# Kernel optimization log

Measured on AMD Instinct MI355X. Metric: run time of the kernel, lower is better.

## Reference

```python
import jax, jax.numpy as jnp
import numpy as np

B, P, ENC = 128, 196, 2048
D, A, ED, V, L = 512, 512, 512, 10000, 20


def setup_inputs() -> dict:
    key = jax.random.key(0)
    ks = jax.random.split(key, 24)
    s = 0.02
    inp = {
        'encoder_out': jax.random.normal(ks[0], (B, P, ENC), jnp.float32),
        'captions': jax.random.randint(ks[1], (B, L), 0, V),
        'caption_len': jax.random.randint(ks[2], (B,), 2, L + 1).at[0].set(L),
        # embedding (uniform(-0.1, 0.1) per init_weights)
        'emb_w': jax.random.uniform(ks[3], (V, ED), jnp.float32, -0.1, 0.1),
        # LSTMCell: input = ED + ENC, hidden = D, gates order i,f,g,o
        'Wih': jax.random.normal(ks[4], (4 * D, ED + ENC), jnp.float32) * s,
        'Whh': jax.random.normal(ks[5], (4 * D, D), jnp.float32) * s,
        'bih': jax.random.normal(ks[6], (4 * D,), jnp.float32) * s,
        'bhh': jax.random.normal(ks[7], (4 * D,), jnp.float32) * s,
        # init hidden state projections
        'h0_w': jax.random.normal(ks[8], (D, ENC), jnp.float32) * s,
        'h0_b': jnp.zeros((D,), jnp.float32),
        'c0_w': jax.random.normal(ks[9], (D, ENC), jnp.float32) * s,
        'c0_b': jnp.zeros((D,), jnp.float32),
        # gate D -> ENC
        'gate_w': jax.random.normal(ks[10], (ENC, D), jnp.float32) * s,
        'gate_b': jnp.zeros((ENC,), jnp.float32),
        # output projection D -> V (uniform(-0.1,0.1), bias 0 per init_weights)
        'lin_w': jax.random.uniform(ks[11], (V, D), jnp.float32, -0.1, 0.1),
        'lin_b': jnp.zeros((V,), jnp.float32),
        # attention network
        'ea_w': jax.random.normal(ks[12], (A, ENC), jnp.float32) * s,
        'ea_b': jnp.zeros((A,), jnp.float32),
        'da_w': jax.random.normal(ks[13], (A, D), jnp.float32) * s,
        'da_b': jnp.zeros((A,), jnp.float32),
        'fa_w': jax.random.normal(ks[14], (1, A), jnp.float32) * s,
        'fa_b': jnp.zeros((1,), jnp.float32),
    }
    return inp


def reference(encoder_out, captions, caption_len, emb_w, Wih, Whh, bih, bhh,
              h0_w, h0_b, c0_w, c0_b, gate_w, gate_b, lin_w, lin_b,
              ea_w, ea_b, da_w, da_b, fa_w, fa_b):
    # sort by caption length descending (as in torch .sort(descending=True))
    order = jnp.argsort(-caption_len)
    cap_len = caption_len[order]
    enc = encoder_out[order]            # [B, P, ENC]
    caps = captions[order]              # [B, L]
    dec_len = cap_len - 1               # per-example decode lengths

    emb = emb_w[caps]                   # [B, L, ED]
    mean_enc = enc.mean(axis=1)         # [B, ENC]
    h0 = mean_enc @ h0_w.T + h0_b       # [B, D]
    c0 = mean_enc @ c0_w.T + c0_b
    att1 = enc @ ea_w.T + ea_b          # [B, P, A] precomputed encoder attention

    T = caps.shape[1] - 1               # static max decode steps (caption_len[0]=L)

    def step(carry, i):
        h, c = carry
        # Bahdanau attention
        att2 = h @ da_w.T + da_b                                   # [B, A]
        e = (jax.nn.relu(att1 + att2[:, None, :]) @ fa_w.T + fa_b)[..., 0]  # [B, P]
        alpha = jax.nn.softmax(e, axis=1)
        awe = jnp.einsum('bp,bpe->be', alpha, enc)                 # [B, ENC]
        g = jax.nn.sigmoid(h @ gate_w.T + gate_b)
        awe = g * awe
        # LSTMCell
        x = jnp.concatenate([emb[:, i, :], awe], axis=1)           # [B, ED+ENC]
        gates = x @ Wih.T + bih + h @ Whh.T + bhh                  # [B, 4D]
        gi, gf, gg, go = jnp.split(gates, 4, axis=1)
        c_new = jax.nn.sigmoid(gf) * c + jax.nn.sigmoid(gi) * jnp.tanh(gg)
        h_new = jax.nn.sigmoid(go) * jnp.tanh(c_new)
        active = (i < dec_len)[:, None]                            # ragged mask
        # inactive rows keep old state (matches h[:batch_size_i] slicing)
        h2 = jnp.where(active, h_new, h)
        c2 = jnp.where(active, c_new, c)
        # dropout is identity in eval; output projection masked to zeros
        pred = jnp.where(active, h_new @ lin_w.T + lin_b, 0.0)     # [B, V]
        alpha = jnp.where(active, alpha, 0.0)
        return (h2, c2), (pred, alpha)

    (_, _), (preds, alphas) = jax.lax.scan(step, (h0, c0), jnp.arange(T))
    pred = jnp.swapaxes(preds, 0, 1)     # [B, T, V]
    alphas = jnp.swapaxes(alphas, 0, 1)  # [B, T, P]
    return pred, caps, dec_len, alphas, order
```

## Files before the change

kernel.cpp:

```cpp
#include <hip/hip_runtime.h>
#include <hip/hip_bf16.h>
#include <math.h>

#define Bn 128
#define Pn 196
#define ENCn 2048
#define Dn 512
#define An 512
#define EDn 512
#define Vn 10000
#define Ln 20
#define Tn 19

typedef short v8s __attribute__((ext_vector_type(8)));
typedef float v4f __attribute__((ext_vector_type(4)));

__device__ __forceinline__ float sigf(float x){ return 1.f/(1.f+__expf(-x)); }
__device__ __forceinline__ unsigned short f2bf(float f){
  unsigned u = __float_as_uint(f);
  return (unsigned short)((u + 0x7FFFu + ((u>>16)&1u)) >> 16);
}
__device__ __forceinline__ float bf2f(unsigned short h){
  return __uint_as_float(((unsigned)h)<<16);
}


__global__ void k_order(const int* __restrict__ caption_len,
                        const int* __restrict__ captions,
                        int* __restrict__ order_i, int* __restrict__ declen_i,
                        int* __restrict__ caps_s,
                        float* __restrict__ out_caps, float* __restrict__ out_declen,
                        float* __restrict__ out_order)
{
  __shared__ int lens[Bn];
  int b = threadIdx.x;
  lens[b] = caption_len[b];
  __syncthreads();
  int lb = lens[b];
  int r = 0;
  for (int j = 0; j < Bn; ++j) {
    int lj = lens[j];
    r += (int)((lj > lb) || (lj == lb && j < b));
  }
  order_i[r] = b;
  declen_i[r] = lb - 1;
  out_order[r] = (float)b;
  out_declen[r] = (float)(lb - 1);
  for (int t = 0; t < Ln; ++t) {
    int cv = captions[b*Ln + t];
    caps_s[r*Ln + t] = cv;
    out_caps[r*Ln + t] = (float)cv;
  }
}

__global__ void k_setup_bias(const float* __restrict__ bih, const float* __restrict__ bhh,
                             const float* __restrict__ da_b, const float* __restrict__ gate_b,
                             const float* __restrict__ h0_b, const float* __restrict__ c0_b,
                             float* __restrict__ bsum_r, float* __restrict__ dg_b,
                             float* __restrict__ hc_b)
{
  int i = blockIdx.x*256 + threadIdx.x;
  if (i < 2048) {
    int d = i >> 2, g = i & 3;
    bsum_r[i] = bih[g*512+d] + bhh[g*512+d];
  }
  if (i < 2560) dg_b[i] = (i < 512) ? da_b[i] : gate_b[i-512];
  if (i < 1024) hc_b[i] = (i < 512) ? h0_b[i] : c0_b[i-512];
}

__global__ void k_cvt(const float* __restrict__ src, unsigned short* __restrict__ dst, int n)
{
  int i = (blockIdx.x*256 + threadIdx.x)*4;
  if (i < n) {
    float4 v = *(const float4*)(src + i);
    dst[i+0]=f2bf(v.x); dst[i+1]=f2bf(v.y); dst[i+2]=f2bf(v.z); dst[i+3]=f2bf(v.w);
  }
}

__global__ void k_wcat(const float* __restrict__ Wih, const float* __restrict__ Whh,
                       unsigned short* __restrict__ dst)
{
  int i = (blockIdx.x*256 + threadIdx.x)*4;
  if (i >= 2048*3072) return;
  int rp = i/3072, j = i - rp*3072;
  int d = rp >> 2, g = rp & 3;
  int r = g*512 + d;
  const float* s = (j < 2560) ? (Wih + (size_t)r*2560 + j) : (Whh + (size_t)r*512 + (j-2560));
  float4 v = *(const float4*)s;
  dst[i+0]=f2bf(v.x); dst[i+1]=f2bf(v.y); dst[i+2]=f2bf(v.z); dst[i+3]=f2bf(v.w);
}

__global__ void k_cvt_enc(const float* __restrict__ enc, const int* __restrict__ order_i,
                          unsigned short* __restrict__ dst)
{
  int id = blockIdx.x;
  int b = id / Pn, p = id - b*Pn;
  const float* src = enc + ((size_t)order_i[b]*Pn + p)*ENCn;
  unsigned short* d = dst + (size_t)id*ENCn;
  int i = threadIdx.x*8;
  float4 v0 = *(const float4*)(src+i), v1 = *(const float4*)(src+i+4);
  d[i+0]=f2bf(v0.x); d[i+1]=f2bf(v0.y); d[i+2]=f2bf(v0.z); d[i+3]=f2bf(v0.w);
  d[i+4]=f2bf(v1.x); d[i+5]=f2bf(v1.y); d[i+6]=f2bf(v1.z); d[i+7]=f2bf(v1.w);
}

__global__ void k_mean(const unsigned short* __restrict__ enc_bf,
                       unsigned short* __restrict__ mean_bf)
{
  int b = blockIdx.x;
  const unsigned short* eb = enc_bf + (size_t)b*Pn*ENCn;
  for (int e = threadIdx.x; e < ENCn; e += 256) {
    float s = 0.f;
    for (int p = 0; p < Pn; ++p) s += bf2f(eb[(size_t)p*ENCn + e]);
    mean_bf[b*ENCn + e] = f2bf(s * (1.f/196.f));
  }
}

__global__ void k_zero(uint4* __restrict__ p, int n)
{
  int i = blockIdx.x*256 + threadIdx.x;
  if (i < n) p[i] = uint4{0,0,0,0};
}

__global__ void k_emb_all(const int* __restrict__ caps_s, const float* __restrict__ emb_w,
                          unsigned short* __restrict__ xh_all)
{
  int id = blockIdx.x; int t = id >> 7, b = id & 127;
  int tok = caps_s[b*Ln + t];
  const float* src = emb_w + (size_t)tok*EDn;
  unsigned short* d = xh_all + ((size_t)t*Bn + b)*3072;
  int i = threadIdx.x*2;
  float2 v = *(const float2*)(src+i);
  d[i] = f2bf(v.x); d[i+1] = f2bf(v.y);
}

__global__ void k_h2bf(const float* __restrict__ hc, float* __restrict__ c,
                       unsigned short* __restrict__ h_bf, unsigned short* __restrict__ xh_all)
{
  int b = blockIdx.x, d = threadIdx.x;
  float hv = hc[b*1024 + d];
  float cv = hc[b*1024 + 512 + d];
  c[b*Dn + d] = cv;
  unsigned short hb = f2bf(hv);
  h_bf[b*Dn + d] = hb;
  xh_all[(size_t)b*3072 + 2560 + d] = hb;
}

template<int MODE, bool OUT_BF16>
__global__ __launch_bounds__(256) void k_mfma_gemm(
    const unsigned short* __restrict__ Aw, const unsigned short* __restrict__ Bw,
    const float* __restrict__ bias, void* __restrict__ Cp,
    int M, int N, int K, size_t ldc,
    const int* __restrict__ actlen, int t)
{
  __shared__ unsigned short smA[2][4096];
  __shared__ unsigned short smB[2][4096];
  const int tid = threadIdx.x;
  int bm0, bn0;
  if constexpr (MODE == 1) {
    int id = blockIdx.x;
    int xcd = id & 7, j = id >> 3;
    int g = j >> 6, rem = j & 63;
    int panel, col;
    if (g < 6) { panel = xcd*49 + g*8 + (rem & 7); col = rem >> 3; }
    else       { panel = xcd*49 + 48;              col = rem; }
    bm0 = panel*64; bn0 = col*64;
  } else {
    bm0 = blockIdx.y*64; bn0 = blockIdx.x*64;
  }

  if (MODE == 0 && actlen && actlen[bm0] <= t) return;

  const int lane = tid & 63, w = tid >> 6;
  const int wr = w >> 1, wc = w & 1;
  const int lrow = lane & 15, kq = lane >> 4;

  v4f acc[2][2];
  #pragma unroll
  for (int i=0;i<2;++i)
    #pragma unroll
    for (int j=0;j<2;++j) acc[i][j] = (v4f)0.f;

  const int nt = K >> 6;

  auto stage = [&](int buf, int k0) {
    #pragma unroll
    for (int it = 0; it < 2; ++it) {
      int s = it*256 + tid;
      int row = s >> 3;
      int kb  = (s & 7) ^ (row & 7);
      {
        const v8s v = *(const v8s*)(Aw + (size_t)(bm0+row)*K + k0 + kb*8);
        *(v8s*)&smA[buf][s*8] = v;
      }
      {
        int gn = bn0 + row; if (gn >= N) gn = N-1;
        const v8s v = *(const v8s*)(Bw + (size_t)gn*K + k0 + kb*8);
        *(v8s*)&smB[buf][s*8] = v;
      }
    }
  };

  auto compute = [&](int buf) {
    #pragma unroll
    for (int kc = 0; kc < 2; ++kc) {
      v8s aF[2], bF[2];
      #pragma unroll
      for (int mi = 0; mi < 2; ++mi) {
        int row = wr*32 + mi*16 + lrow;
        int kb = kc*4 + kq;
        aF[mi] = *(const v8s*)&smA[buf][row*64 + ((kb ^ (row&7))<<3)];
      }
      #pragma unroll
      for (int ni = 0; ni < 2; ++ni) {
        int row = wc*32 + ni*16 + lrow;
        int kb = kc*4 + kq;
        bF[ni] = *(const v8s*)&smB[buf][row*64 + ((kb ^ (row&7))<<3)];
      }
      #pragma unroll
      for (int mi = 0; mi < 2; ++mi)
        #pragma unroll
        for (int ni = 0; ni < 2; ++ni)
          acc[mi][ni] = __builtin_amdgcn_mfma_f32_16x16x32_bf16(aF[mi], bF[ni], acc[mi][ni], 0, 0, 0);
    }
  };

  stage(0, 0);
  __syncthreads();
  for (int tk = 0; tk < nt; ++tk) {
    if (tk + 1 < nt) stage((tk+1)&1, (tk+1)<<6);
    compute(tk&1);
    __syncthreads();
  }

  #pragma unroll
  for (int mi=0; mi<2; ++mi)
    #pragma unroll
    for (int ni=0; ni<2; ++ni) {
      #pragma unroll
      for (int r=0; r<4; ++r) {
        int m = bm0 + wr*32 + mi*16 + kq*4 + r;
        int n = bn0 + wc*32 + ni*16 + lrow;
        if (m < M && n < N) {
          float v = acc[mi][ni][r] + (bias ? bias[n] : 0.f);
          if constexpr (OUT_BF16) ((unsigned short*)Cp)[(size_t)m*ldc + n] = f2bf(v);
          else ((float*)Cp)[(size_t)m*ldc + n] = v;
        }
      }
    }
}

__global__ __launch_bounds__(256) void k_gates_lstm(
    const unsigned short* __restrict__ Aw, const unsigned short* __restrict__ Bw,
    const float* __restrict__ bias,
    float* __restrict__ c, unsigned short* __restrict__ h_bf,
    unsigned short* __restrict__ h_all, unsigned short* __restrict__ xh_all,
    const int* __restrict__ declen_i, int t)
{
  __shared__ unsigned short smA[2][4096];
  __shared__ unsigned short smB[2][4096];
  __shared__ float smC[64][65];
  const int tid = threadIdx.x;
  const int bm0 = blockIdx.y*64, bn0 = blockIdx.x*64;
  if (declen_i[bm0] <= t) return;

  const int lane = tid & 63, w = tid >> 6;
  const int wr = w >> 1, wc = w & 1;
  const int lrow = lane & 15, kq = lane >> 4;
  const int K = 3072;

  v4f acc[2][2];
  #pragma unroll
  for (int i=0;i<2;++i)
    #pragma unroll
    for (int j=0;j<2;++j) acc[i][j] = (v4f)0.f;

  auto stage = [&](int buf, int k0) {
    #pragma unroll
    for (int it = 0; it < 2; ++it) {
      int s = it*256 + tid;
      int row = s >> 3;
      int kb  = (s & 7) ^ (row & 7);
      *(v8s*)&smA[buf][s*8] = *(const v8s*)(Aw + (size_t)(bm0+row)*K + k0 + kb*8);
      *(v8s*)&smB[buf][s*8] = *(const v8s*)(Bw + (size_t)(bn0+row)*K + k0 + kb*8);
    }
  };
  auto compute = [&](int buf) {
    #pragma unroll
    for (int kc = 0; kc < 2; ++kc) {
      v8s aF[2], bF[2];
      #pragma unroll
      for (int mi = 0; mi < 2; ++mi) {
        int row = wr*32 + mi*16 + lrow;
        int kb = kc*4 + kq;
        aF[mi] = *(const v8s*)&smA[buf][row*64 + ((kb ^ (row&7))<<3)];
      }
      #pragma unroll
      for (int ni = 0; ni < 2; ++ni) {
        int row = wc*32 + ni*16 + lrow;
        int kb = kc*4 + kq;
        bF[ni] = *(const v8s*)&smB[buf][row*64 + ((kb ^ (row&7))<<3)];
      }
      #pragma unroll
      for (int mi = 0; mi < 2; ++mi)
        #pragma unroll
        for (int ni = 0; ni < 2; ++ni)
          acc[mi][ni] = __builtin_amdgcn_mfma_f32_16x16x32_bf16(aF[mi], bF[ni], acc[mi][ni], 0, 0, 0);
    }
  };

  stage(0, 0);
  __syncthreads();
  const int nt = K >> 6;
  for (int tk = 0; tk < nt; ++tk) {
    if (tk + 1 < nt) stage((tk+1)&1, (tk+1)<<6);
    compute(tk&1);
    __syncthreads();
  }

  #pragma unroll
  for (int mi=0; mi<2; ++mi)
    #pragma unroll
    for (int ni=0; ni<2; ++ni)
      #pragma unroll
      for (int r=0; r<4; ++r) {
        int ml = wr*32 + mi*16 + kq*4 + r;
        int nl = wc*32 + ni*16 + lrow;
        smC[ml][nl] = acc[mi][ni][r] + bias[bn0 + nl];
      }
  __syncthreads();

  for (int idx = tid; idx < 1024; idx += 256) {
    int ml = idx >> 4, dl = idx & 15;
    int b = bm0 + ml;
    if (t < declen_i[b]) {
      int dg = (bn0 >> 2) + dl;
      float gi = smC[ml][dl*4+0];
      float gf = smC[ml][dl*4+1];
      float gg = smC[ml][dl*4+2];
      float go = smC[ml][dl*4+3];
      float cv = c[b*Dn + dg];
      float cn = sigf(gf)*cv + sigf(gi)*tanhf(gg);
      float hn = sigf(go)*tanhf(cn);
      c[b*Dn + dg] = cn;
      unsigned short hb = f2bf(hn);
      h_bf[b*Dn + dg] = hb;
      h_all[((size_t)t*Bn + b)*Dn + dg] = hb;
      if (t + 1 < Tn)
        xh_all[((size_t)(t+1)*Bn + b)*3072 + 2560 + dg] = hb;
    }
  }
}

__global__ __launch_bounds__(256) void k_pred(
    const unsigned short* __restrict__ Aw, const unsigned short* __restrict__ Bw,
    const float* __restrict__ bias, float* __restrict__ out_pred,
    const int* __restrict__ declen_i)
{
  __shared__ unsigned short smA[2][4096];
  __shared__ unsigned short smB[2][4096];
  const int tid = threadIdx.x;
  const int bm0 = blockIdx.y*64, bn0 = blockIdx.x*64;
  const int t0 = bm0 >> 7, b0 = bm0 & 127;

  if (declen_i[b0] <= t0) {
    for (int i = tid; i < 4096; i += 256) {
      int ml = i >> 6, nl = i & 63;
      int n = bn0 + nl;
      if (n < Vn) {
        int m = bm0 + ml;
        out_pred[((size_t)(m & 127)*Tn + (m >> 7))*Vn + n] = 0.f;
      }
    }
    return;
  }

  const int lane = tid & 63, w = tid >> 6;
  const int wr = w >> 1, wc = w & 1;
  const int lrow = lane & 15, kq = lane >> 4;
  const int K = 512;

  v4f acc[2][2];
  #pragma unroll
  for (int i=0;i<2;++i)
    #pragma unroll
    for (int j=0;j<2;++j) acc[i][j] = (v4f)0.f;

  auto stage = [&](int buf, int k0) {
    #pragma unroll
    for (int it = 0; it < 2; ++it) {
      int s = it*256 + tid;
      int row = s >> 3;
      int kb  = (s & 7) ^ (row & 7);
      *(v8s*)&smA[buf][s*8] = *(const v8s*)(Aw + (size_t)(bm0+row)*K + k0 + kb*8);
      {
        int gn = bn0 + row; if (gn >= Vn) gn = Vn-1;
        *(v8s*)&smB[buf][s*8] = *(const v8s*)(Bw + (size_t)gn*K + k0 + kb*8);
      }
    }
  };
  auto compute = [&](int buf) {
    #pragma unroll
    for (int kc = 0; kc < 2; ++kc) {
      v8s aF[2], bF[2];
      #pragma unroll
      for (int mi = 0; mi < 2; ++mi) {
        int row = wr*32 + mi*16 + lrow;
        int kb = kc*4 + kq;
        aF[mi] = *(const v8s*)&smA[buf][row*64 + ((kb ^ (row&7))<<3)];
      }
      #pragma unroll
      for (int ni = 0; ni < 2; ++ni) {
        int row = wc*32 + ni*16 + lrow;
        int kb = kc*4 + kq;
        bF[ni] = *(const v8s*)&smB[buf][row*64 + ((kb ^ (row&7))<<3)];
      }
      #pragma unroll
      for (int mi = 0; mi < 2; ++mi)
        #pragma unroll
        for (int ni = 0; ni < 2; ++ni)
          acc[mi][ni] = __builtin_amdgcn_mfma_f32_16x16x32_bf16(aF[mi], bF[ni], acc[mi][ni], 0, 0, 0);
    }
  };

  stage(0, 0);
  __syncthreads();
  const int nt = K >> 6;
  for (int tk = 0; tk < nt; ++tk) {
    if (tk + 1 < nt) stage((tk+1)&1, (tk+1)<<6);
    compute(tk&1);
    __syncthreads();
  }

  #pragma unroll
  for (int mi=0; mi<2; ++mi)
    #pragma unroll
    for (int ni=0; ni<2; ++ni)
      #pragma unroll
      for (int r=0; r<4; ++r) {
        int m = bm0 + wr*32 + mi*16 + kq*4 + r;
        int n = bn0 + wc*32 + ni*16 + lrow;
        if (n < Vn) {
          int b = m & 127, tt = m >> 7;
          float v = (tt < declen_i[b]) ? (acc[mi][ni][r] + bias[n]) : 0.f;
          out_pred[((size_t)b*Tn + tt)*Vn + n] = v;
        }
      }
}

__global__ __launch_bounds__(256) void k_esm(
    const unsigned short* __restrict__ att1, const float* __restrict__ att2g,
    const float* __restrict__ fa_w, const float* __restrict__ fa_b,
    float* __restrict__ alpha, float* __restrict__ out_alph,
    const int* __restrict__ declen_i, int t)
{
  int b = blockIdx.x;
  int tid = threadIdx.x;
  if (t >= declen_i[b]) {
    if (tid < Pn)
      out_alph[(size_t)b*Tn*Pn + (size_t)t*Pn + tid] = 0.f;
    return;
  }
  __shared__ float a2s[An];
  __shared__ float fws[An];
  __shared__ float es[Pn];
  __shared__ float wred[4];
  __shared__ float wsum[4];
  for (int i = tid; i < An; i += 256) { a2s[i] = att2g[(size_t)b*2560 + i]; fws[i] = fa_w[i]; }
  __syncthreads();
  int lane = tid & 63, w = tid >> 6;
  if (tid < Pn) {
    const unsigned short* row = att1 + ((size_t)b*Pn + tid)*An;
    float s = 0.f;
    #pragma unroll 4
    for (int kb = 0; kb < 64; ++kb) {
      const v8s vv = *(const v8s*)(row + kb*8);
      #pragma unroll
      for (int j = 0; j < 8; ++j) {
        int a = kb*8 + j;
        float v = bf2f((unsigned short)vv[j]) + a2s[a];
        s += fmaxf(v, 0.f) * fws[a];
      }
    }
    es[tid] = s + fa_b[0];
  }
  __syncthreads();
  float m = -1e30f;
  for (int p = tid; p < Pn; p += 256) m = fmaxf(m, es[p]);
  for (int off = 32; off; off >>= 1) m = fmaxf(m, __shfl_down(m, off));
  if (lane == 0) wred[w] = m;
  __syncthreads();
  m = fmaxf(fmaxf(wred[0], wred[1]), fmaxf(wred[2], wred[3]));
  float s = 0.f;
  for (int p = tid; p < Pn; p += 256) { float ev = __expf(es[p] - m); es[p] = ev; s += ev; }
  for (int off = 32; off; off >>= 1) s += __shfl_down(s, off);
  if (lane == 0) wsum[w] = s;
  __syncthreads();
  s = wsum[0] + wsum[1] + wsum[2] + wsum[3];
  float inv = 1.f / s;
  for (int p = tid; p < Pn; p += 256) {
    float al = es[p] * inv;
    alpha[b*Pn + p] = al;
    out_alph[(size_t)b*Tn*Pn + (size_t)t*Pn + p] = al;
  }
}

__global__ __launch_bounds__(256) void k_awe_gate(
    const unsigned short* __restrict__ enc_bf,
    const float* __restrict__ alpha, const float* __restrict__ att2g,
    unsigned short* __restrict__ xh_t, const int* __restrict__ declen_i, int t)
{
  int b = blockIdx.y;
  if (t >= declen_i[b]) return;
  __shared__ float als[Pn];
  __shared__ float red[8][256];
  int tid = threadIdx.x;
  if (tid < Pn) als[tid] = alpha[b*Pn + tid];
  __syncthreads();
  int e0 = blockIdx.x*256;
  int ec = tid & 31, ps = tid >> 5;
  const unsigned short* eb = enc_bf + (size_t)b*Pn*ENCn + e0 + ec*8;
  float s[8] = {};
  for (int p = ps; p < Pn; p += 8) {
    v8s v = *(const v8s*)(eb + (size_t)p*ENCn);
    float a = als[p];
    #pragma unroll
    for (int j = 0; j < 8; ++j) s[j] += a * bf2f((unsigned short)v[j]);
  }
  #pragma unroll
  for (int j = 0; j < 8; ++j) red[ps][ec*8+j] = s[j];
  __syncthreads();
  {
    int e = tid;
    float tsum = 0.f;
    #pragma unroll
    for (int k = 0; k < 8; ++k) tsum += red[k][e];
    int eg = e0 + e;
    float g = sigf(att2g[(size_t)b*2560 + 512 + eg]);
    xh_t[(size_t)b*3072 + 512 + eg] = f2bf(g*tsum);
  }
}


extern "C" void kernel_launch(void* const* d_in, const int* in_sizes, int n_in,
                              void* d_out, int out_size, void* d_ws, size_t ws_size,
                              hipStream_t stream)
{
  const float* enc     = (const float*)d_in[0];
  const int*   captions= (const int*)d_in[1];
  const int*   cap_len = (const int*)d_in[2];
  const float* emb_w   = (const float*)d_in[3];
  const float* Wih     = (const float*)d_in[4];
  const float* Whh     = (const float*)d_in[5];
  const float* bih     = (const float*)d_in[6];
  const float* bhh     = (const float*)d_in[7];
  const float* h0_w    = (const float*)d_in[8];
  const float* h0_b    = (const float*)d_in[9];
  const float* c0_w    = (const float*)d_in[10];
  const float* c0_b    = (const float*)d_in[11];
  const float* gate_w  = (const float*)d_in[12];
  const float* gate_b  = (const float*)d_in[13];
  const float* lin_w   = (const float*)d_in[14];
  const float* lin_b   = (const float*)d_in[15];
  const float* ea_w    = (const float*)d_in[16];
  const float* ea_b    = (const float*)d_in[17];
  const float* da_w    = (const float*)d_in[18];
  const float* da_b    = (const float*)d_in[19];
  const float* fa_w    = (const float*)d_in[20];
  const float* fa_b    = (const float*)d_in[21];

  float* out = (float*)d_out;
  float* out_pred   = out;
  float* out_caps   = out + (size_t)Bn*Tn*Vn;
  float* out_declen = out_caps + Bn*Ln;
  float* out_alph   = out_declen + Bn;
  float* out_order  = out_alph + (size_t)Bn*Tn*Pn;

  char* wp = (char*)d_ws;
  auto alloc = [&](size_t bytes)->void* {
    void* p = (void*)wp; wp += (bytes + 255) & ~(size_t)255; return p;
  };
  int*   order_i  = (int*)alloc(Bn*4);
  int*   declen_i = (int*)alloc(Bn*4);
  int*   caps_s   = (int*)alloc(Bn*Ln*4);
  unsigned short* enc_bf  = (unsigned short*)alloc((size_t)Bn*Pn*ENCn*2);
  unsigned short* mean_bf = (unsigned short*)alloc((size_t)Bn*ENCn*2);
  float* hc       = (float*)alloc((size_t)Bn*1024*4);
  float* c        = (float*)alloc((size_t)Bn*Dn*4);
  unsigned short* h_bf   = (unsigned short*)alloc((size_t)Bn*Dn*2);
  unsigned short* h_all  = (unsigned short*)alloc((size_t)Tn*Bn*Dn*2);
  unsigned short* xh_all = (unsigned short*)alloc((size_t)Tn*Bn*3072*2);
  unsigned short* att1   = (unsigned short*)alloc((size_t)Bn*Pn*An*2);
  float* att2g    = (float*)alloc((size_t)Bn*2560*4);
  float* alpha    = (float*)alloc((size_t)Bn*Pn*4);
  unsigned short* ea_bf   = (unsigned short*)alloc((size_t)An*ENCn*2);
  unsigned short* lin_bf  = (unsigned short*)alloc((size_t)Vn*Dn*2);
  unsigned short* h0c0_bf = (unsigned short*)alloc((size_t)1024*ENCn*2);
  unsigned short* dg_bf   = (unsigned short*)alloc((size_t)2560*Dn*2);
  unsigned short* wcat_bf = (unsigned short*)alloc((size_t)2048*3072*2);
  float* bsum = (float*)alloc(2048*4);
  float* dg_b = (float*)alloc(2560*4);
  float* hc_b = (float*)alloc(1024*4);

  k_order<<<1,128,0,stream>>>(cap_len, captions, order_i, declen_i, caps_s,
                              out_caps, out_declen, out_order);
  k_setup_bias<<<10,256,0,stream>>>(bih, bhh, da_b, gate_b, h0_b, c0_b, bsum, dg_b, hc_b);
  k_cvt<<<(An*ENCn/4+255)/256,256,0,stream>>>(ea_w, ea_bf, An*ENCn);
  k_cvt<<<(Vn*Dn/4+255)/256,256,0,stream>>>(lin_w, lin_bf, Vn*Dn);
  k_cvt<<<(Dn*ENCn/4+255)/256,256,0,stream>>>(h0_w, h0c0_bf, Dn*ENCn);
  k_cvt<<<(Dn*ENCn/4+255)/256,256,0,stream>>>(c0_w, h0c0_bf + (size_t)512*ENCn, Dn*ENCn);
  k_cvt<<<(An*Dn/4+255)/256,256,0,stream>>>(da_w, dg_bf, An*Dn);
  k_cvt<<<(ENCn*Dn/4+255)/256,256,0,stream>>>(gate_w, dg_bf + (size_t)512*Dn, ENCn*Dn);
  k_wcat<<<(2048*3072/4+255)/256,256,0,stream>>>(Wih, Whh, wcat_bf);
  k_cvt_enc<<<Bn*Pn,256,0,stream>>>(enc, order_i, enc_bf);
  k_mean<<<Bn,256,0,stream>>>(enc_bf, mean_bf);
  k_zero<<<((int)((size_t)Tn*Bn*3072*2/16)+255)/256,256,0,stream>>>(
      (uint4*)xh_all, (int)((size_t)Tn*Bn*3072*2/16));
  k_emb_all<<<Tn*Bn,256,0,stream>>>(caps_s, emb_w, xh_all);

  k_mfma_gemm<0,false><<<dim3(16,2),256,0,stream>>>(
      mean_bf, h0c0_bf, hc_b, hc, Bn, 1024, ENCn, 1024, nullptr, 0);
  k_h2bf<<<Bn,512,0,stream>>>(hc, c, h_bf, xh_all);

  k_mfma_gemm<1,true><<<dim3(392*8),256,0,stream>>>(
      enc_bf, ea_bf, ea_b, att1, Bn*Pn, An, ENCn, An, nullptr, 0);

  for (int t = 0; t < Tn; ++t) {
    unsigned short* xh_t = xh_all + (size_t)t*Bn*3072;
    k_mfma_gemm<0,false><<<dim3(40,2),256,0,stream>>>(
        h_bf, dg_bf, dg_b, att2g, Bn, 2560, Dn, 2560, declen_i, t);
    k_esm<<<Bn,256,0,stream>>>(att1, att2g, fa_w, fa_b, alpha, out_alph, declen_i, t);
    k_awe_gate<<<dim3(8,Bn),256,0,stream>>>(enc_bf, alpha, att2g, xh_t, declen_i, t);
    k_gates_lstm<<<dim3(32,2),256,0,stream>>>(
        xh_t, wcat_bf, bsum, c, h_bf, h_all, xh_all, declen_i, t);
  }

  k_pred<<<dim3((Vn+63)/64, (Tn*Bn)/64),256,0,stream>>>(
      h_all, lin_bf, lin_b, out_pred, declen_i);
}
```

Measured before the change: 1.697 ms.

## Fuse per-step decoder-attention and gate GEMV into softmax and AWE kernels

Removes the per-timestep MFMA GEMM that computed att2 and the gate pre-activation into a global buffer. Each k_esm block now computes its own batch row's 512-wide decoder attention projection, and each k_awe_gate block computes its slice of the sigmoid gate, both as scalar GEMVs over bf16 weights. This drops one launch and one global round trip per step, at the cost of redundant weight reads across the batch blocks and non-tensor-core arithmetic. Separately, the one-time att1 GEMM moves to a dedicated kernel with 128x64 tiles and its own XCD-aware block mapping.

Measured after the change: 2.358 ms. +38.9%, slower.

```diff
diff --git a/kernel.cpp b/kernel.cpp
--- a/kernel.cpp
+++ b/kernel.cpp
@@ -145,30 +145,15 @@
   xh_all[(size_t)b*3072 + 2560 + d] = hb;
 }
 
-template<int MODE, bool OUT_BF16>
 __global__ __launch_bounds__(256) void k_mfma_gemm(
     const unsigned short* __restrict__ Aw, const unsigned short* __restrict__ Bw,
-    const float* __restrict__ bias, void* __restrict__ Cp,
-    int M, int N, int K, size_t ldc,
-    const int* __restrict__ actlen, int t)
+    const float* __restrict__ bias, float* __restrict__ Cp,
+    int N, int K, size_t ldc)
 {
   __shared__ unsigned short smA[2][4096];
   __shared__ unsigned short smB[2][4096];
   const int tid = threadIdx.x;
-  int bm0, bn0;
-  if constexpr (MODE == 1) {
-    int id = blockIdx.x;
-    int xcd = id & 7, j = id >> 3;
-    int g = j >> 6, rem = j & 63;
-    int panel, col;
-    if (g < 6) { panel = xcd*49 + g*8 + (rem & 7); col = rem >> 3; }
-    else       { panel = xcd*49 + 48;              col = rem; }
-    bm0 = panel*64; bn0 = col*64;
-  } else {
-    bm0 = blockIdx.y*64; bn0 = blockIdx.x*64;
-  }
-
-  if (MODE == 0 && actlen && actlen[bm0] <= t) return;
+  const int bm0 = blockIdx.y*64, bn0 = blockIdx.x*64;
 
   const int lane = tid & 63, w = tid >> 6;
   const int wr = w >> 1, wc = w & 1;
@@ -188,18 +173,10 @@
       int s = it*256 + tid;
       int row = s >> 3;
       int kb  = (s & 7) ^ (row & 7);
-      {
-        const v8s v = *(const v8s*)(Aw + (size_t)(bm0+row)*K + k0 + kb*8);
-        *(v8s*)&smA[buf][s*8] = v;
-      }
-      {
-        int gn = bn0 + row; if (gn >= N) gn = N-1;
-        const v8s v = *(const v8s*)(Bw + (size_t)gn*K + k0 + kb*8);
-        *(v8s*)&smB[buf][s*8] = v;
-      }
-    }
-  };
-
+      *(v8s*)&smA[buf][s*8] = *(const v8s*)(Aw + (size_t)(bm0+row)*K + k0 + kb*8);
+      *(v8s*)&smB[buf][s*8] = *(const v8s*)(Bw + (size_t)(bn0+row)*K + k0 + kb*8);
+    }
+  };
   auto compute = [&](int buf) {
     #pragma unroll
     for (int kc = 0; kc < 2; ++kc) {
@@ -235,18 +212,96 @@
   #pragma unroll
   for (int mi=0; mi<2; ++mi)
     #pragma unroll
-    for (int ni=0; ni<2; ++ni) {
+    for (int ni=0; ni<2; ++ni)
       #pragma unroll
       for (int r=0; r<4; ++r) {
         int m = bm0 + wr*32 + mi*16 + kq*4 + r;
         int n = bn0 + wc*32 + ni*16 + lrow;
-        if (m < M && n < N) {
-          float v = acc[mi][ni][r] + (bias ? bias[n] : 0.f);
-          if constexpr (OUT_BF16) ((unsigned short*)Cp)[(size_t)m*ldc + n] = f2bf(v);
-          else ((float*)Cp)[(size_t)m*ldc + n] = v;
-        }
-      }
-    }
+        Cp[(size_t)m*ldc + n] = acc[mi][ni][r] + bias[n];
+      }
+}
+
+__global__ __launch_bounds__(256) void k_att1(
+    const unsigned short* __restrict__ Aw, const unsigned short* __restrict__ Bw,
+    const float* __restrict__ bias, unsigned short* __restrict__ Cp)
+{
+  __shared__ unsigned short smA[2][8192];
+  __shared__ unsigned short smB[2][4096];
+  const int tid = threadIdx.x;
+  const int id = blockIdx.x;
+  const int g = (id & 7)*196 + (id >> 3);
+  const int bm0 = (g >> 3) * 128, bn0 = (g & 7) * 64;
+  const int K = ENCn;
+
+  const int lane = tid & 63, w = tid >> 6;
+  const int wr = w >> 1, wc = w & 1;
+  const int lrow = lane & 15, kq = lane >> 4;
+
+  v4f acc[4][2];
+  #pragma unroll
+  for (int i=0;i<4;++i)
+    #pragma unroll
+    for (int j=0;j<2;++j) acc[i][j] = (v4f)0.f;
+
+  auto stage = [&](int buf, int k0) {
+    #pragma unroll
+    for (int it = 0; it < 4; ++it) {
+      int s = it*256 + tid;
+      int row = s >> 3;
+      int kb  = (s & 7) ^ (row & 7);
+      *(v8s*)&smA[buf][s*8] = *(const v8s*)(Aw + (size_t)(bm0+row)*K + k0 + kb*8);
+    }
+    #pragma unroll
+    for (int it = 0; it < 2; ++it) {
+      int s = it*256 + tid;
+      int row = s >> 3;
+      int kb  = (s & 7) ^ (row & 7);
+      *(v8s*)&smB[buf][s*8] = *(const v8s*)(Bw + (size_t)(bn0+row)*K + k0 + kb*8);
+    }
+  };
+  auto compute = [&](int buf) {
+    #pragma unroll
+    for (int kc = 0; kc < 2; ++kc) {
+      v8s aF[4], bF[2];
+      #pragma unroll
+      for (int mi = 0; mi < 4; ++mi) {
+        int row = wr*64 + mi*16 + lrow;
+        int kb = kc*4 + kq;
+        aF[mi] = *(const v8s*)&smA[buf][row*64 + ((kb ^ (row&7))<<3)];
+      }
+      #pragma unroll
+      for (int ni = 0; ni < 2; ++ni) {
+        int row = wc*32 + ni*16 + lrow;
+        int kb = kc*4 + kq;
+        bF[ni] = *(const v8s*)&smB[buf][row*64 + ((kb ^ (row&7))<<3)];
+      }
+      #pragma unroll
+      for (int mi = 0; mi < 4; ++mi)
+        #pragma unroll
+        for (int ni = 0; ni < 2; ++ni)
+          acc[mi][ni] = __builtin_amdgcn_mfma_f32_16x16x32_bf16(aF[mi], bF[ni], acc[mi][ni], 0, 0, 0);
+    }
+  };
+
+  stage(0, 0);
+  __syncthreads();
+  const int nt = K >> 6;
+  for (int tk = 0; tk < nt; ++tk) {
+    if (tk + 1 < nt) stage((tk+1)&1, (tk+1)<<6);
+    compute(tk&1);
+    __syncthreads();
+  }
+
+  #pragma unroll
+  for (int mi=0; mi<4; ++mi)
+    #pragma unroll
+    for (int ni=0; ni<2; ++ni)
+      #pragma unroll
+      for (int r=0; r<4; ++r) {
+        int m = bm0 + wr*64 + mi*16 + kq*4 + r;
+        int n = bn0 + wc*32 + ni*16 + lrow;
+        Cp[(size_t)m*An + n] = f2bf(acc[mi][ni][r] + bias[n]);
+      }
 }
 
 __global__ __launch_bounds__(256) void k_gates_lstm(
@@ -448,7 +503,8 @@
 }
 
 __global__ __launch_bounds__(256) void k_esm(
-    const unsigned short* __restrict__ att1, const float* __restrict__ att2g,
+    const unsigned short* __restrict__ att1, const unsigned short* __restrict__ dg_bf,
+    const float* __restrict__ dg_b, const unsigned short* __restrict__ h_bf,
     const float* __restrict__ fa_w, const float* __restrict__ fa_b,
     float* __restrict__ alpha, float* __restrict__ out_alph,
     const int* __restrict__ declen_i, int t)
@@ -460,28 +516,52 @@
       out_alph[(size_t)b*Tn*Pn + (size_t)t*Pn + tid] = 0.f;
     return;
   }
+  __shared__ float h_l[Dn];
   __shared__ float a2s[An];
   __shared__ float fws[An];
   __shared__ float es[Pn];
   __shared__ float wred[4];
   __shared__ float wsum[4];
-  for (int i = tid; i < An; i += 256) { a2s[i] = att2g[(size_t)b*2560 + i]; fws[i] = fa_w[i]; }
+  for (int i = tid; i < Dn; i += 256) h_l[i] = bf2f(h_bf[b*Dn + i]);
+  for (int i = tid; i < An; i += 256) fws[i] = fa_w[i];
+  __syncthreads();
+  #pragma unroll
+  for (int i = 0; i < 2; ++i) {
+    int n = tid + i*256;
+    const unsigned short* row = dg_bf + (size_t)n*Dn;
+    float s0=0.f, s1=0.f, s2=0.f, s3=0.f;
+    for (int kb = 0; kb < 64; kb += 4) {
+      #pragma unroll
+      for (int u = 0; u < 4; ++u) {
+        v8s v = *(const v8s*)(row + (kb+u)*8);
+        float s = 0.f;
+        #pragma unroll
+        for (int j = 0; j < 8; ++j) s += bf2f((unsigned short)v[j]) * h_l[(kb+u)*8+j];
+        if (u==0) s0 += s; else if (u==1) s1 += s; else if (u==2) s2 += s; else s3 += s;
+      }
+    }
+    a2s[n] = s0+s1+s2+s3 + dg_b[n];
+  }
   __syncthreads();
   int lane = tid & 63, w = tid >> 6;
   if (tid < Pn) {
     const unsigned short* row = att1 + ((size_t)b*Pn + tid)*An;
-    float s = 0.f;
-    #pragma unroll 4
-    for (int kb = 0; kb < 64; ++kb) {
-      const v8s vv = *(const v8s*)(row + kb*8);
-      #pragma unroll
-      for (int j = 0; j < 8; ++j) {
-        int a = kb*8 + j;
-        float v = bf2f((unsigned short)vv[j]) + a2s[a];
-        s += fmaxf(v, 0.f) * fws[a];
-      }
-    }
-    es[tid] = s + fa_b[0];
+    float s0=0.f, s1=0.f, s2=0.f, s3=0.f;
+    for (int kb = 0; kb < 64; kb += 4) {
+      #pragma unroll
+      for (int u = 0; u < 4; ++u) {
+        const v8s vv = *(const v8s*)(row + (kb+u)*8);
+        float s = 0.f;
+        #pragma unroll
+        for (int j = 0; j < 8; ++j) {
+          int a = (kb+u)*8 + j;
+          float v = bf2f((unsigned short)vv[j]) + a2s[a];
+          s += fmaxf(v, 0.f) * fws[a];
+        }
+        if (u==0) s0 += s; else if (u==1) s1 += s; else if (u==2) s2 += s; else s3 += s;
+      }
+    }
+    es[tid] = s0+s1+s2+s3 + fa_b[0];
   }
   __syncthreads();
   float m = -1e30f;
@@ -505,18 +585,38 @@
 }
 
 __global__ __launch_bounds__(256) void k_awe_gate(
-    const unsigned short* __restrict__ enc_bf,
-    const float* __restrict__ alpha, const float* __restrict__ att2g,
+    const unsigned short* __restrict__ enc_bf, const unsigned short* __restrict__ dg_bf,
+    const float* __restrict__ dg_b, const unsigned short* __restrict__ h_bf,
+    const float* __restrict__ alpha,
     unsigned short* __restrict__ xh_t, const int* __restrict__ declen_i, int t)
 {
   int b = blockIdx.y;
   if (t >= declen_i[b]) return;
+  __shared__ float h_l[Dn];
   __shared__ float als[Pn];
+  __shared__ float gp[256];
   __shared__ float red[8][256];
   int tid = threadIdx.x;
+  for (int i = tid; i < Dn; i += 256) h_l[i] = bf2f(h_bf[b*Dn + i]);
   if (tid < Pn) als[tid] = alpha[b*Pn + tid];
   __syncthreads();
   int e0 = blockIdx.x*256;
+  {
+    int eg = e0 + tid;
+    const unsigned short* row = dg_bf + (size_t)(512 + eg)*Dn;
+    float s0=0.f, s1=0.f, s2=0.f, s3=0.f;
+    for (int kb = 0; kb < 64; kb += 4) {
+      #pragma unroll
+      for (int u = 0; u < 4; ++u) {
+        v8s v = *(const v8s*)(row + (kb+u)*8);
+        float s = 0.f;
+        #pragma unroll
+        for (int j = 0; j < 8; ++j) s += bf2f((unsigned short)v[j]) * h_l[(kb+u)*8+j];
+        if (u==0) s0 += s; else if (u==1) s1 += s; else if (u==2) s2 += s; else s3 += s;
+      }
+    }
+    gp[tid] = sigf(s0+s1+s2+s3 + dg_b[512 + eg]);
+  }
   int ec = tid & 31, ps = tid >> 5;
   const unsigned short* eb = enc_bf + (size_t)b*Pn*ENCn + e0 + ec*8;
   float s[8] = {};
@@ -530,13 +630,10 @@
   for (int j = 0; j < 8; ++j) red[ps][ec*8+j] = s[j];
   __syncthreads();
   {
-    int e = tid;
     float tsum = 0.f;
     #pragma unroll
-    for (int k = 0; k < 8; ++k) tsum += red[k][e];
-    int eg = e0 + e;
-    float g = sigf(att2g[(size_t)b*2560 + 512 + eg]);
-    xh_t[(size_t)b*3072 + 512 + eg] = f2bf(g*tsum);
+    for (int k = 0; k < 8; ++k) tsum += red[k][tid];
+    xh_t[(size_t)b*3072 + 512 + e0 + tid] = f2bf(gp[tid]*tsum);
   }
 }
 
@@ -590,7 +687,6 @@
   unsigned short* h_all  = (unsigned short*)alloc((size_t)Tn*Bn*Dn*2);
   unsigned short* xh_all = (unsigned short*)alloc((size_t)Tn*Bn*3072*2);
   unsigned short* att1   = (unsigned short*)alloc((size_t)Bn*Pn*An*2);
-  float* att2g    = (float*)alloc((size_t)Bn*2560*4);
   float* alpha    = (float*)alloc((size_t)Bn*Pn*4);
   unsigned short* ea_bf   = (unsigned short*)alloc((size_t)An*ENCn*2);
   unsigned short* lin_bf  = (unsigned short*)alloc((size_t)Vn*Dn*2);
@@ -617,19 +713,18 @@
       (uint4*)xh_all, (int)((size_t)Tn*Bn*3072*2/16));
   k_emb_all<<<Tn*Bn,256,0,stream>>>(caps_s, emb_w, xh_all);
 
-  k_mfma_gemm<0,false><<<dim3(16,2),256,0,stream>>>(
-      mean_bf, h0c0_bf, hc_b, hc, Bn, 1024, ENCn, 1024, nullptr, 0);
+  k_mfma_gemm<<<dim3(16,2),256,0,stream>>>(
+      mean_bf, h0c0_bf, hc_b, hc, 1024, ENCn, 1024);
   k_h2bf<<<Bn,512,0,stream>>>(hc, c, h_bf, xh_all);
 
-  k_mfma_gemm<1,true><<<dim3(392*8),256,0,stream>>>(
-      enc_bf, ea_bf, ea_b, att1, Bn*Pn, An, ENCn, An, nullptr, 0);
+  k_att1<<<dim3(196*8),256,0,stream>>>(enc_bf, ea_bf, ea_b, att1);
 
   for (int t = 0; t < Tn; ++t) {
     unsigned short* xh_t = xh_all + (size_t)t*Bn*3072;
-    k_mfma_gemm<0,false><<<dim3(40,2),256,0,stream>>>(
-        h_bf, dg_bf, dg_b, att2g, Bn, 2560, Dn, 2560, declen_i, t);
-    k_esm<<<Bn,256,0,stream>>>(att1, att2g, fa_w, fa_b, alpha, out_alph, declen_i, t);
-    k_awe_gate<<<dim3(8,Bn),256,0,stream>>>(enc_bf, alpha, att2g, xh_t, declen_i, t);
+    k_esm<<<Bn,256,0,stream>>>(att1, dg_bf, dg_b, h_bf, fa_w, fa_b,
+                               alpha, out_alph, declen_i, t);
+    k_awe_gate<<<dim3(8,Bn),256,0,stream>>>(enc_bf, dg_bf, dg_b, h_bf,
+                                            alpha, xh_t, declen_i, t);
     k_gates_lstm<<<dim3(32,2),256,0,stream>>>(
         xh_t, wcat_bf, bsum, c, h_bf, h_all, xh_all, declen_i, t);
   }
```
